# Kernel optimization log

Measured on AMD Instinct MI355X. Metric: run time of the kernel, lower is better.

The kernel has to match this reference:

```python
import jax, jax.numpy as jnp
import numpy as np

MAX_NUM_CAPS = 10
NEG = -1e9

def _layernorm(x, g, b):
    m = x.mean(-1, keepdims=True)
    v = x.var(-1, keepdims=True)
    return (x - m) / jnp.sqrt(v + 1e-5) * g + b

def _gatv2(x, Wl, Wr, att, bias, adj):
    # x: [B,M,F]; Wl/Wr: [F,H*C]; att: [H,C]; adj: [B,M,M] bool, adj[b,i,j] = edge i->j
    B, M, F = x.shape
    H, C = att.shape
    xl = jnp.einsum('bmf,fhc->bmhc', x, Wl.reshape(F, H, C))  # source transform
    xr = jnp.einsum('bmf,fhc->bmhc', x, Wr.reshape(F, H, C))  # target transform
    # GATv2 score: att . leaky_relu(xl[i] + xr[j]) for edge (src=i, dst=j)
    z = jax.nn.leaky_relu(xl[:, :, None, :, :] + xr[:, None, :, :, :], 0.2)  # [B,i,j,H,C]
    e = jnp.einsum('bijhc,hc->bijh', z, att)
    e = jnp.where(adj[..., None], e, NEG)
    alpha = jax.nn.softmax(e, axis=1)  # softmax over incoming sources i per target j
    out = jnp.einsum('bijh,bihc->bjhc', alpha, xl)  # aggregate at targets
    return out.reshape(B, M, H * C) + bias

def setup_inputs() -> dict:
    key = jax.random.key(0)
    ks = jax.random.split(key, 16)
    B, N, T = 128, 16, 48
    Fm, H, C3 = 128, 4, 64
    s = 0.05
    inp = {
        'team_obs': jax.random.normal(ks[0], (B, N, 14), jnp.float32),
        'target_obs': jax.random.normal(ks[1], (B, T, 15), jnp.float32),
        'team_mask': jax.random.normal(ks[2], (B, 2, N), jnp.float32),
        'local_target_mask': jnp.ones((B, T + 1), jnp.float32),
        'W_emb': jax.random.normal(ks[3], (16, Fm), jnp.float32) * s,
        'b_emb': jnp.zeros((Fm,), jnp.float32),
        'Wl1': jax.random.normal(ks[4], (Fm, Fm), jnp.float32) * s,
        'Wr1': jax.random.normal(ks[5], (Fm, Fm), jnp.float32) * s,
        'att1': jax.random.normal(ks[6], (H, Fm // H), jnp.float32) * s,
        'b1': jnp.zeros((Fm,), jnp.float32),
        'Wl2': jax.random.normal(ks[7], (Fm, Fm), jnp.float32) * s,
        'Wr2': jax.random.normal(ks[8], (Fm, Fm), jnp.float32) * s,
        'att2': jax.random.normal(ks[9], (H, Fm // H), jnp.float32) * s,
        'b2': jnp.zeros((Fm,), jnp.float32),
        'Wl3': jax.random.normal(ks[10], (Fm, C3), jnp.float32) * s,
        'Wr3': jax.random.normal(ks[11], (Fm, C3), jnp.float32) * s,
        'att3': jax.random.normal(ks[12], (1, C3), jnp.float32) * s,
        'b3': jnp.zeros((C3,), jnp.float32),
        'ln1_g': jnp.ones((Fm,), jnp.float32),
        'ln1_b': jnp.zeros((Fm,), jnp.float32),
        'ln2_g': jnp.ones((Fm,), jnp.float32),
        'ln2_b': jnp.zeros((Fm,), jnp.float32),
    }
    return inp

def reference(team_obs, target_obs, team_mask, local_target_mask,
              W_emb, b_emb, Wl1, Wr1, att1, b1, Wl2, Wr2, att2, b2,
              Wl3, Wr3, att3, b3, ln1_g, ln1_b, ln2_g, ln2_b):
    B, N, _ = team_obs.shape
    team = jnp.concatenate([team_obs, jnp.zeros((B, N, 2), team_obs.dtype)], axis=2)
    tgt = target_obs[:, :, :-1]
    T = tgt.shape[1]
    tgt = jnp.concatenate([tgt[:, :, :2 + MAX_NUM_CAPS],
                           jnp.zeros((B, T, 2), tgt.dtype),
                           tgt[:, :, -2:]], axis=2)
    fin = jnp.concatenate([team, tgt], axis=1)  # [B, M, inp_dim]
    h = fin @ W_emb + b_emb  # [B, M, 128]
    imp_team = team_mask[:, 0] != -1e9          # [B, N]
    imp_tgt = local_target_mask[:, :-1] != 0.0  # [B, T]
    imp = jnp.concatenate([imp_team, imp_tgt], axis=1)  # [B, M]
    M = N + T
    eye = jnp.eye(M, dtype=bool)
    # edges among active nodes minus diagonal; PyG GATv2Conv add_self_loops=True re-adds self edges
    adj = (imp[:, :, None] & imp[:, None, :] & ~eye) | eye  # [B, M, M]
    out = jax.nn.relu(_layernorm(_gatv2(h, Wl1, Wr1, att1, b1, adj), ln1_g, ln1_b))
    out = jax.nn.relu(_layernorm(_gatv2(out, Wl2, Wr2, att2, b2, adj), ln2_g, ln2_b))
    out = _gatv2(out, Wl3, Wr3, att3, b3, adj)
    return out  # [B, M, out_dim]
```

## Files before the change

### kernel.cpp

```cpp
#include <hip/hip_runtime.h>

typedef unsigned short u16;
typedef unsigned int   u32;
typedef _Float16 h2  __attribute__((ext_vector_type(2)));
typedef __fp16   hw2 __attribute__((ext_vector_type(2)));

#define XS 136

static __device__ __forceinline__ h2 pk(float a, float b) {
    return __builtin_bit_cast(h2, __builtin_amdgcn_cvt_pkrtz(a, b));
}
static __device__ __forceinline__ float dot2(h2 a, h2 b, float c) {
    return __builtin_amdgcn_fdot2(__builtin_bit_cast(hw2, a),
                                  __builtin_bit_cast(hw2, b), c, false);
}
static __device__ __forceinline__ h2  b2h(u32 v) { return __builtin_bit_cast(h2, v); }
static __device__ __forceinline__ u32 h2u(h2 v)  { return __builtin_bit_cast(u32, v); }
static __device__ __forceinline__ h2  abs2(h2 v) { return b2h(h2u(v) & 0x7fff7fffu); }
static __device__ __forceinline__ u16 f2h(float f) { return __builtin_bit_cast(u16, (_Float16)f); }
static __device__ __forceinline__ float h2f(u16 v) { return (float)__builtin_bit_cast(_Float16, v); }

__global__ void pack_weights(const float* __restrict__ Wl1, const float* __restrict__ Wr1,
                             const float* __restrict__ Wl2, const float* __restrict__ Wr2,
                             const float* __restrict__ Wl3, const float* __restrict__ Wr3,
                             u32* __restrict__ wpk)
{
    const int blk = blockIdx.x, t = threadIdx.x;
    const float* src; u32* dst; int local; int sh;
    if      (blk < 32)  { src = Wl1; dst = wpk;         local = blk*256 + t;       sh = 7; }
    else if (blk < 64)  { src = Wr1; dst = wpk + 8192;  local = (blk-32)*256 + t;  sh = 7; }
    else if (blk < 96)  { src = Wl2; dst = wpk + 16384; local = (blk-64)*256 + t;  sh = 7; }
    else if (blk < 128) { src = Wr2; dst = wpk + 24576; local = (blk-96)*256 + t;  sh = 7; }
    else if (blk < 144) { src = Wl3; dst = wpk + 32768; local = (blk-128)*256 + t; sh = 6; }
    else                { src = Wr3; dst = wpk + 36864; local = (blk-144)*256 + t; sh = 6; }
    const int N  = 1 << sh;
    const int k2 = local >> sh;
    const int n  = local & (N - 1);
    float a = src[(2*k2)*N + n];
    float b = src[(2*k2+1)*N + n];
    dst[local] = h2u(pk(a, b));
}

static __device__ __forceinline__ void gat_layer(
    int t, int w, int lane,
    const u32* __restrict__ wpkL, const u32* __restrict__ wpkR,
    const float* __restrict__ att, const float* __restrict__ bias,
    const float* __restrict__ lg, const float* __restrict__ lb,
    u16* sX, u16* sXl, u16* sXrT, float* sAl, float* sPart, float* sL2, const float* sImp)
{
    {
        const int n = t & 127;
        const int g = t >> 7;
        float accL[16], accR[16];
#pragma unroll
        for (int q = 0; q < 16; q++) { accL[q] = 0.f; accR[q] = 0.f; }
        for (int kb = 0; kb < 16; kb++) {
            h2 wl2[4], wr2[4];
#pragma unroll
            for (int q = 0; q < 4; q++) {
                int k2 = kb*4 + q;
                wl2[q] = b2h(wpkL[k2*128 + n]);
                wr2[q] = b2h(wpkR[k2*128 + n]);
            }
#pragma unroll
            for (int mm = 0; mm < 16; mm++) {
                int m = g*16 + mm;
                uint4 v = *(const uint4*)&sX[m*XS + kb*8];
                h2 x0 = b2h(v.x), x1 = b2h(v.y), x2 = b2h(v.z), x3 = b2h(v.w);
                accL[mm] = dot2(x0, wl2[0], accL[mm]);
                accL[mm] = dot2(x1, wl2[1], accL[mm]);
                accL[mm] = dot2(x2, wl2[2], accL[mm]);
                accL[mm] = dot2(x3, wl2[3], accL[mm]);
                accR[mm] = dot2(x0, wr2[0], accR[mm]);
                accR[mm] = dot2(x1, wr2[1], accR[mm]);
                accR[mm] = dot2(x2, wr2[2], accR[mm]);
                accR[mm] = dot2(x3, wr2[3], accR[mm]);
            }
        }
#pragma unroll
        for (int mm = 0; mm < 16; mm++) {
            int m = g*16 + mm;
            sXl[m*XS + n]  = f2h(accL[mm]);
            sXrT[n*65 + m] = f2h(accR[mm]);
        }
    }
    __syncthreads();

    const int h     = w & 3;
    const int ihalf = w >> 2;
    const int j     = lane;

    h2 a2[16];
#pragma unroll
    for (int q = 0; q < 16; q++) a2[q] = pk(att[h*32 + 2*q], att[h*32 + 2*q + 1]);

    if (w < 4) {
        const uint4* pr = (const uint4*)&sXl[lane*XS + h*32];
        float al = 0.f;
#pragma unroll
        for (int c4 = 0; c4 < 4; c4++) {
            uint4 v = pr[c4];
            al = dot2(b2h(v.x), a2[c4*4+0], al);
            al = dot2(b2h(v.y), a2[c4*4+1], al);
            al = dot2(b2h(v.z), a2[c4*4+2], al);
            al = dot2(b2h(v.w), a2[c4*4+3], al);
        }
        sAl[h*64 + lane] = al;
    }

    h2 xr2[16];
#pragma unroll
    for (int q = 0; q < 16; q++) {
        int c = h*32 + 2*q;
        u16 r0 = sXrT[c*65 + j];
        u16 r1 = sXrT[(c+1)*65 + j];
        xr2[q] = b2h((u32)r0 | ((u32)r1 << 16));
    }
    float Ar = 0.f;
#pragma unroll
    for (int q = 0; q < 16; q++) Ar = dot2(a2[q], xr2[q], Ar);
    const float impj = sImp[j];
    __syncthreads();

    float l = 0.f;
    h2 acc2[16];
#pragma unroll
    for (int q = 0; q < 16; q++) acc2[q] = b2h(0u);
    const int i0 = ihalf * 32;
#pragma unroll 4
    for (int ii = 0; ii < 32; ii++) {
        int i = i0 + ii;
        const uint4* pl = (const uint4*)&sXl[i*XS + h*32];
        uint4 v0 = pl[0], v1 = pl[1], v2 = pl[2], v3 = pl[3];
        h2 xl2[16];
        xl2[0] = b2h(v0.x); xl2[1] = b2h(v0.y); xl2[2]  = b2h(v0.z); xl2[3]  = b2h(v0.w);
        xl2[4] = b2h(v1.x); xl2[5] = b2h(v1.y); xl2[6]  = b2h(v1.z); xl2[7]  = b2h(v1.w);
        xl2[8] = b2h(v2.x); xl2[9] = b2h(v2.y); xl2[10] = b2h(v2.z); xl2[11] = b2h(v2.w);
        xl2[12]= b2h(v3.x); xl2[13]= b2h(v3.y); xl2[14] = b2h(v3.z); xl2[15] = b2h(v3.w);
        float S0 = 0.f, S1 = 0.f;
#pragma unroll
        for (int q = 0; q < 16; q += 2) {
            h2 t0 = abs2(xl2[q]   + xr2[q]);
            h2 t1 = abs2(xl2[q+1] + xr2[q+1]);
            S0 = dot2(a2[q],   t0, S0);
            S1 = dot2(a2[q+1], t1, S1);
        }
        float e  = 0.6f*(sAl[h*64 + i] + Ar) + 0.4f*(S0 + S1);
        float ad = (i == j) ? 1.f : impj * sImp[i];
        float p  = (ad != 0.f) ? __expf(e) : 0.f;
        l += p;
        h2 p2 = pk(p, p);
#pragma unroll
        for (int q = 0; q < 16; q++) acc2[q] += p2 * xl2[q];
    }

    u32* ov = (u32*)sX;
    if (w >= 4) {
        uint4* d4 = (uint4*)(ov + (h*64 + j)*16);
        uint4 o;
        o.x = h2u(acc2[0]);  o.y = h2u(acc2[1]);  o.z = h2u(acc2[2]);  o.w = h2u(acc2[3]);  d4[0] = o;
        o.x = h2u(acc2[4]);  o.y = h2u(acc2[5]);  o.z = h2u(acc2[6]);  o.w = h2u(acc2[7]);  d4[1] = o;
        o.x = h2u(acc2[8]);  o.y = h2u(acc2[9]);  o.z = h2u(acc2[10]); o.w = h2u(acc2[11]); d4[2] = o;
        o.x = h2u(acc2[12]); o.y = h2u(acc2[13]); o.z = h2u(acc2[14]); o.w = h2u(acc2[15]); d4[3] = o;
        sL2[h*64 + j] = l;
    }
    __syncthreads();

    float yv[32];
    if (w < 4) {
        const uint4* s4 = (const uint4*)(ov + (h*64 + j)*16);
        uint4 u0 = s4[0], u1 = s4[1], u2 = s4[2], u3 = s4[3];
        h2 oth[16];
        oth[0] = b2h(u0.x); oth[1] = b2h(u0.y); oth[2]  = b2h(u0.z); oth[3]  = b2h(u0.w);
        oth[4] = b2h(u1.x); oth[5] = b2h(u1.y); oth[6]  = b2h(u1.z); oth[7]  = b2h(u1.w);
        oth[8] = b2h(u2.x); oth[9] = b2h(u2.y); oth[10] = b2h(u2.z); oth[11] = b2h(u2.w);
        oth[12]= b2h(u3.x); oth[13]= b2h(u3.y); oth[14] = b2h(u3.z); oth[15] = b2h(u3.w);
        l += sL2[h*64 + j];
        const float rl = 1.f / l;
        float s1 = 0.f, s2v = 0.f;
#pragma unroll
        for (int q = 0; q < 16; q++) {
            h2 sum = acc2[q] + oth[q];
            float y0 = fmaf((float)sum[0], rl, bias[h*32 + 2*q]);
            float y1 = fmaf((float)sum[1], rl, bias[h*32 + 2*q + 1]);
            yv[2*q] = y0; yv[2*q+1] = y1;
            s1 += y0 + y1;
            s2v = fmaf(y0, y0, s2v);
            s2v = fmaf(y1, y1, s2v);
        }
        sPart[h*64 + j]       = s1;
        sPart[256 + h*64 + j] = s2v;
    }
    __syncthreads();

    if (w < 4) {
        float su = sPart[j] + sPart[64 + j] + sPart[128 + j] + sPart[192 + j];
        float sq = sPart[256 + j] + sPart[320 + j] + sPart[384 + j] + sPart[448 + j];
        const float mean = su * 0.0078125f;
        const float var  = sq * 0.0078125f - mean*mean;
        const float rstd = rsqrtf(var + 1e-5f);
        u32* xd = (u32*)&sX[j*XS + h*32];
#pragma unroll
        for (int q = 0; q < 16; q++) {
            int f0 = h*32 + 2*q;
            float v0 = fmaxf(fmaf((yv[2*q]   - mean)*rstd, lg[f0],   lb[f0]),   0.f);
            float v1 = fmaxf(fmaf((yv[2*q+1] - mean)*rstd, lg[f0+1], lb[f0+1]), 0.f);
            xd[q] = h2u(pk(v0, v1));
        }
    }
    __syncthreads();
}

__global__ void __launch_bounds__(512, 2) GNN_61040075210810_kernel(
    const float* __restrict__ team_obs, const float* __restrict__ target_obs,
    const float* __restrict__ team_mask, const float* __restrict__ local_target_mask,
    const float* __restrict__ W_emb, const float* __restrict__ b_emb,
    const float* __restrict__ att1, const float* __restrict__ b1,
    const float* __restrict__ att2, const float* __restrict__ b2,
    const float* __restrict__ att3, const float* __restrict__ b3,
    const float* __restrict__ ln1_g, const float* __restrict__ ln1_b,
    const float* __restrict__ ln2_g, const float* __restrict__ ln2_b,
    const u32* __restrict__ wpk,
    float* __restrict__ out)
{
    __shared__ __align__(16) u16 sX  [64*XS];
    __shared__ __align__(16) u16 sXl [64*XS];
    __shared__ __align__(16) u16 sXrT[128*65];
    __shared__ float sFin[1024];
    __shared__ float sAl [256];
    __shared__ float sPart[512];
    __shared__ float sL2 [256];
    __shared__ float sImp[64];

    const int t    = threadIdx.x;
    const int w    = t >> 6;
    const int lane = t & 63;
    const int b    = blockIdx.x;

    if (t < 64) {
        float im;
        if (t < 16) im = (team_mask[b*32 + t] != -1000000000.0f) ? 1.f : 0.f;
        else        im = (local_target_mask[b*49 + (t-16)] != 0.0f) ? 1.f : 0.f;
        sImp[t] = im;
    }
    for (int ee = t; ee < 1024; ee += 512) {
        int m = ee >> 4, k = ee & 15;
        float v = 0.f;
        if (m < 16) {
            if (k < 14) v = team_obs[(b*16 + m)*14 + k];
        } else {
            const float* tg = target_obs + (size_t)(b*48 + (m-16))*15;
            if      (k < 12)  v = tg[k];
            else if (k == 14) v = tg[12];
            else if (k == 15) v = tg[13];
        }
        sFin[m*16 + k] = v;
    }
    __syncthreads();

    {
        const int f = t & 127;
        const int g = t >> 7;
        float wreg[16];
#pragma unroll
        for (int k = 0; k < 16; k++) wreg[k] = W_emb[k*128 + f];
        const float bf = b_emb[f];
#pragma unroll
        for (int mm = 0; mm < 16; mm++) {
            int m = g*16 + mm;
            const float4* pf = (const float4*)&sFin[m*16];
            float4 f0 = pf[0], f1 = pf[1], f2 = pf[2], f3 = pf[3];
            float acc = bf;
            acc = fmaf(f0.x, wreg[0],  acc); acc = fmaf(f0.y, wreg[1],  acc);
            acc = fmaf(f0.z, wreg[2],  acc); acc = fmaf(f0.w, wreg[3],  acc);
            acc = fmaf(f1.x, wreg[4],  acc); acc = fmaf(f1.y, wreg[5],  acc);
            acc = fmaf(f1.z, wreg[6],  acc); acc = fmaf(f1.w, wreg[7],  acc);
            acc = fmaf(f2.x, wreg[8],  acc); acc = fmaf(f2.y, wreg[9],  acc);
            acc = fmaf(f2.z, wreg[10], acc); acc = fmaf(f2.w, wreg[11], acc);
            acc = fmaf(f3.x, wreg[12], acc); acc = fmaf(f3.y, wreg[13], acc);
            acc = fmaf(f3.z, wreg[14], acc); acc = fmaf(f3.w, wreg[15], acc);
            sX[m*XS + f] = f2h(acc);
        }
    }
    __syncthreads();

    gat_layer(t, w, lane, wpk,         wpk + 8192,  att1, b1, ln1_g, ln1_b,
              sX, sXl, sXrT, sAl, sPart, sL2, sImp);
    gat_layer(t, w, lane, wpk + 16384, wpk + 24576, att2, b2, ln2_g, ln2_b,
              sX, sXl, sXrT, sAl, sPart, sL2, sImp);

    {
        const int col = t & 63;
        const int isR = (t >> 6) & 1;
        const int g   = t >> 7;
        const u32* wp = isR ? (wpk + 36864) : (wpk + 32768);
        float acc[16];
#pragma unroll
        for (int q = 0; q < 16; q++) acc[q] = 0.f;
        for (int kb = 0; kb < 16; kb++) {
            h2 w2[4];
#pragma unroll
            for (int q = 0; q < 4; q++) w2[q] = b2h(wp[(kb*4 + q)*64 + col]);
#pragma unroll
            for (int mm = 0; mm < 16; mm++) {
                int m = g*16 + mm;
                uint4 v = *(const uint4*)&sX[m*XS + kb*8];
                acc[mm] = dot2(b2h(v.x), w2[0], acc[mm]);
                acc[mm] = dot2(b2h(v.y), w2[1], acc[mm]);
                acc[mm] = dot2(b2h(v.z), w2[2], acc[mm]);
                acc[mm] = dot2(b2h(v.w), w2[3], acc[mm]);
            }
        }
#pragma unroll
        for (int mm = 0; mm < 16; mm++) {
            int m = g*16 + mm;
            if (isR) sXrT[col*65 + m] = f2h(acc[mm]);
            else     sXl[m*XS + col]  = f2h(acc[mm]);
        }
    }
    __syncthreads();

    {
        h2 a2l[4];
#pragma unroll
        for (int q = 0; q < 4; q++) a2l[q] = pk(att3[w*8 + 2*q], att3[w*8 + 2*q + 1]);
        uint4 v = *(const uint4*)&sXl[lane*XS + w*8];
        float al = 0.f;
        al = dot2(b2h(v.x), a2l[0], al);
        al = dot2(b2h(v.y), a2l[1], al);
        al = dot2(b2h(v.z), a2l[2], al);
        al = dot2(b2h(v.w), a2l[3], al);
        sPart[w*64 + lane] = al;
    }
    __syncthreads();
    if (t < 64) {
        sAl[t] = ((sPart[t] + sPart[64+t]) + (sPart[128+t] + sPart[192+t]))
               + ((sPart[256+t] + sPart[320+t]) + (sPart[384+t] + sPart[448+t]));
    }
    __syncthreads();

    const int j = lane;
    u16* sE = &sXrT[64*65];

    {
        h2 a3[32], xr3[32];
#pragma unroll
        for (int q = 0; q < 32; q++) a3[q] = pk(att3[2*q], att3[2*q + 1]);
#pragma unroll
        for (int q = 0; q < 32; q++) {
            u16 r0 = sXrT[(2*q)*65 + j];
            u16 r1 = sXrT[(2*q + 1)*65 + j];
            xr3[q] = b2h((u32)r0 | ((u32)r1 << 16));
        }
        float Ar = 0.f;
#pragma unroll
        for (int q = 0; q < 32; q++) Ar = dot2(a3[q], xr3[q], Ar);
        const float impj = sImp[j];
        const int i0 = w*8;
        for (int ii = 0; ii < 8; ii++) {
            int i = i0 + ii;
            const uint4* pl = (const uint4*)&sXl[i*XS];
            float S0 = 0.f, S1 = 0.f;
#pragma unroll
            for (int c4 = 0; c4 < 8; c4++) {
                uint4 v = pl[c4];
                S0 = dot2(a3[c4*4+0], abs2(b2h(v.x) + xr3[c4*4+0]), S0);
                S1 = dot2(a3[c4*4+1], abs2(b2h(v.y) + xr3[c4*4+1]), S1);
                S0 = dot2(a3[c4*4+2], abs2(b2h(v.z) + xr3[c4*4+2]), S0);
                S1 = dot2(a3[c4*4+3], abs2(b2h(v.w) + xr3[c4*4+3]), S1);
            }
            float e  = 0.6f*(sAl[i] + Ar) + 0.4f*(S0 + S1);
            float ad = (i == j) ? 1.f : impj * sImp[i];
            e = (ad != 0.f) ? e : -60000.0f;
            sE[i*64 + j] = f2h(e);
        }
    }
    __syncthreads();

    {
        const int c0 = w*8;
        h2 acc2[4];
#pragma unroll
        for (int q = 0; q < 4; q++) acc2[q] = b2h(0u);
        float l = 0.f;
        for (int i = 0; i < 64; i++) {
            float p = __expf(h2f(sE[i*64 + j]));
            l += p;
            h2 p2 = pk(p, p);
            uint4 v = *(const uint4*)&sXl[i*XS + c0];
            acc2[0] += p2 * b2h(v.x);
            acc2[1] += p2 * b2h(v.y);
            acc2[2] += p2 * b2h(v.z);
            acc2[3] += p2 * b2h(v.w);
        }
        const float rl = 1.f / l;
        float o[8];
#pragma unroll
        for (int q = 0; q < 4; q++) {
            o[2*q]   = fmaf((float)acc2[q][0], rl, b3[c0 + 2*q]);
            o[2*q+1] = fmaf((float)acc2[q][1], rl, b3[c0 + 2*q + 1]);
        }
        float4* po = (float4*)(out + (size_t)b*4096 + j*64 + c0);
        po[0] = *(const float4*)&o[0];
        po[1] = *(const float4*)&o[4];
    }
}

extern "C" void kernel_launch(void* const* d_in, const int* in_sizes, int n_in,
                              void* d_out, int out_size, void* d_ws, size_t ws_size,
                              hipStream_t stream) {
    (void)in_sizes; (void)n_in; (void)ws_size; (void)out_size;
    const float* team_obs          = (const float*)d_in[0];
    const float* target_obs        = (const float*)d_in[1];
    const float* team_mask         = (const float*)d_in[2];
    const float* local_target_mask = (const float*)d_in[3];
    const float* W_emb             = (const float*)d_in[4];
    const float* b_emb             = (const float*)d_in[5];
    const float* Wl1               = (const float*)d_in[6];
    const float* Wr1               = (const float*)d_in[7];
    const float* att1              = (const float*)d_in[8];
    const float* b1                = (const float*)d_in[9];
    const float* Wl2               = (const float*)d_in[10];
    const float* Wr2               = (const float*)d_in[11];
    const float* att2              = (const float*)d_in[12];
    const float* b2                = (const float*)d_in[13];
    const float* Wl3               = (const float*)d_in[14];
    const float* Wr3               = (const float*)d_in[15];
    const float* att3              = (const float*)d_in[16];
    const float* b3                = (const float*)d_in[17];
    const float* ln1_g             = (const float*)d_in[18];
    const float* ln1_b             = (const float*)d_in[19];
    const float* ln2_g             = (const float*)d_in[20];
    const float* ln2_b             = (const float*)d_in[21];
    float* out = (float*)d_out;
    u32*   wpk = (u32*)d_ws;

    pack_weights<<<dim3(160), dim3(256), 0, stream>>>(Wl1, Wr1, Wl2, Wr2, Wl3, Wr3, wpk);
    GNN_61040075210810_kernel<<<dim3(128), dim3(512), 0, stream>>>(
        team_obs, target_obs, team_mask, local_target_mask, W_emb, b_emb,
        att1, b1, att2, b2, att3, b3, ln1_g, ln1_b, ln2_g, ln2_b, wpk, out);
}
```

Baseline: 161.8 us.

## Use MFMA 16x16x32 f16 for GAT linear projections with fragment-packed weights

Result: faster. 144.8 us (-10.5%).

```diff
diff --git a/kernel.cpp b/kernel.cpp
--- a/kernel.cpp
+++ b/kernel.cpp
@@ -4,6 +4,8 @@
 typedef unsigned int   u32;
 typedef _Float16 h2  __attribute__((ext_vector_type(2)));
 typedef __fp16   hw2 __attribute__((ext_vector_type(2)));
+typedef __fp16   hw8 __attribute__((ext_vector_type(8)));
+typedef float    f4  __attribute__((ext_vector_type(4)));
 
 #define XS 136
 
@@ -19,26 +21,32 @@
 static __device__ __forceinline__ h2  abs2(h2 v) { return b2h(h2u(v) & 0x7fff7fffu); }
 static __device__ __forceinline__ u16 f2h(float f) { return __builtin_bit_cast(u16, (_Float16)f); }
 static __device__ __forceinline__ float h2f(u16 v) { return (float)__builtin_bit_cast(_Float16, v); }
+static __device__ __forceinline__ f4 mfma16(uint4 a, uint4 b, f4 c) {
+    return __builtin_amdgcn_mfma_f32_16x16x32_f16(__builtin_bit_cast(hw8, a),
+                                                  __builtin_bit_cast(hw8, b), c, 0, 0, 0);
+}
 
 __global__ void pack_weights(const float* __restrict__ Wl1, const float* __restrict__ Wr1,
                              const float* __restrict__ Wl2, const float* __restrict__ Wr2,
                              const float* __restrict__ Wl3, const float* __restrict__ Wr3,
                              u32* __restrict__ wpk)
 {
-    const int blk = blockIdx.x, t = threadIdx.x;
-    const float* src; u32* dst; int local; int sh;
-    if      (blk < 32)  { src = Wl1; dst = wpk;         local = blk*256 + t;       sh = 7; }
-    else if (blk < 64)  { src = Wr1; dst = wpk + 8192;  local = (blk-32)*256 + t;  sh = 7; }
-    else if (blk < 96)  { src = Wl2; dst = wpk + 16384; local = (blk-64)*256 + t;  sh = 7; }
-    else if (blk < 128) { src = Wr2; dst = wpk + 24576; local = (blk-96)*256 + t;  sh = 7; }
-    else if (blk < 144) { src = Wl3; dst = wpk + 32768; local = (blk-128)*256 + t; sh = 6; }
-    else                { src = Wr3; dst = wpk + 36864; local = (blk-144)*256 + t; sh = 6; }
-    const int N  = 1 << sh;
-    const int k2 = local >> sh;
-    const int n  = local & (N - 1);
-    float a = src[(2*k2)*N + n];
-    float b = src[(2*k2+1)*N + n];
-    dst[local] = h2u(pk(a, b));
+    const int o = blockIdx.x * 256 + threadIdx.x;
+    const float* src; u32* dst; int local; int N;
+    if      (o < 8192)  { src = Wl1; dst = wpk;         local = o;         N = 128; }
+    else if (o < 16384) { src = Wr1; dst = wpk + 8192;  local = o - 8192;  N = 128; }
+    else if (o < 24576) { src = Wl2; dst = wpk + 16384; local = o - 16384; N = 128; }
+    else if (o < 32768) { src = Wr2; dst = wpk + 24576; local = o - 24576; N = 128; }
+    else if (o < 36864) { src = Wl3; dst = wpk + 32768; local = o - 32768; N = 64;  }
+    else                { src = Wr3; dst = wpk + 36864; local = o - 36864; N = 64;  }
+    const int i2   = local & 3;
+    const int lane = (local >> 2) & 63;
+    const int frag = local >> 8;
+    const int kb   = frag & 3;
+    const int nt   = frag >> 2;
+    const int k0   = kb*32 + ((lane >> 4) << 3) + i2*2;
+    const int n    = nt*16 + (lane & 15);
+    dst[local] = h2u(pk(src[k0*N + n], src[(k0+1)*N + n]));
 }
 
 static __device__ __forceinline__ void gat_layer(
@@ -46,42 +54,37 @@
     const u32* __restrict__ wpkL, const u32* __restrict__ wpkR,
     const float* __restrict__ att, const float* __restrict__ bias,
     const float* __restrict__ lg, const float* __restrict__ lb,
-    u16* sX, u16* sXl, u16* sXrT, float* sAl, float* sPart, float* sL2, const float* sImp)
+    u16* sX, u16* sXl, uint4* sXrP, float* sAl, float* sPart, float* sL2, const float* sImp)
 {
     {
-        const int n = t & 127;
-        const int g = t >> 7;
-        float accL[16], accR[16];
-#pragma unroll
-        for (int q = 0; q < 16; q++) { accL[q] = 0.f; accR[q] = 0.f; }
-        for (int kb = 0; kb < 16; kb++) {
-            h2 wl2[4], wr2[4];
-#pragma unroll
-            for (int q = 0; q < 4; q++) {
-                int k2 = kb*4 + q;
-                wl2[q] = b2h(wpkL[k2*128 + n]);
-                wr2[q] = b2h(wpkR[k2*128 + n]);
+        const int  mt  = w & 3;
+        const bool isR = (w >= 4);
+        const u32* wp  = isR ? wpkR : wpkL;
+        const int  n15 = lane & 15;
+        const int  qd  = lane >> 4;
+        uint4 afr[4];
+#pragma unroll
+        for (int kb = 0; kb < 4; kb++)
+            afr[kb] = *(const uint4*)&sX[(mt*16 + n15)*XS + kb*32 + (qd << 3)];
+#pragma unroll
+        for (int nt = 0; nt < 8; nt++) {
+            f4 acc = {0.f, 0.f, 0.f, 0.f};
+#pragma unroll
+            for (int kb = 0; kb < 4; kb++) {
+                uint4 bf = *(const uint4*)&wp[((nt*4 + kb)*64 + lane)*4];
+                acc = mfma16(afr[kb], bf, acc);
             }
-#pragma unroll
-            for (int mm = 0; mm < 16; mm++) {
-                int m = g*16 + mm;
-                uint4 v = *(const uint4*)&sX[m*XS + kb*8];
-                h2 x0 = b2h(v.x), x1 = b2h(v.y), x2 = b2h(v.z), x3 = b2h(v.w);
-                accL[mm] = dot2(x0, wl2[0], accL[mm]);
-                accL[mm] = dot2(x1, wl2[1], accL[mm]);
-                accL[mm] = dot2(x2, wl2[2], accL[mm]);
-                accL[mm] = dot2(x3, wl2[3], accL[mm]);
-                accR[mm] = dot2(x0, wr2[0], accR[mm]);
-                accR[mm] = dot2(x1, wr2[1], accR[mm]);
-                accR[mm] = dot2(x2, wr2[2], accR[mm]);
-                accR[mm] = dot2(x3, wr2[3], accR[mm]);
+            const int n  = nt*16 + n15;
+            const int mb = mt*16 + (qd << 2);
+            if (!isR) {
+#pragma unroll
+                for (int r = 0; r < 4; r++) sXl[(mb + r)*XS + n] = f2h(acc[r]);
+            } else {
+                u16* xp = (u16*)sXrP;
+#pragma unroll
+                for (int r = 0; r < 4; r++)
+                    xp[(((n >> 3)*64) + mb + r)*8 + (n & 7)] = f2h(acc[r]);
             }
-        }
-#pragma unroll
-        for (int mm = 0; mm < 16; mm++) {
-            int m = g*16 + mm;
-            sXl[m*XS + n]  = f2h(accL[mm]);
-            sXrT[n*65 + m] = f2h(accR[mm]);
         }
     }
     __syncthreads();
@@ -110,11 +113,10 @@
 
     h2 xr2[16];
 #pragma unroll
-    for (int q = 0; q < 16; q++) {
-        int c = h*32 + 2*q;
-        u16 r0 = sXrT[c*65 + j];
-        u16 r1 = sXrT[(c+1)*65 + j];
-        xr2[q] = b2h((u32)r0 | ((u32)r1 << 16));
+    for (int s = 0; s < 4; s++) {
+        uint4 v = sXrP[(h*4 + s)*64 + j];
+        xr2[s*4+0] = b2h(v.x); xr2[s*4+1] = b2h(v.y);
+        xr2[s*4+2] = b2h(v.z); xr2[s*4+3] = b2h(v.w);
     }
     float Ar = 0.f;
 #pragma unroll
@@ -223,9 +225,9 @@
     const u32* __restrict__ wpk,
     float* __restrict__ out)
 {
-    __shared__ __align__(16) u16 sX  [64*XS];
-    __shared__ __align__(16) u16 sXl [64*XS];
-    __shared__ __align__(16) u16 sXrT[128*65];
+    __shared__ __align__(16) u16   sX  [64*XS];
+    __shared__ __align__(16) u16   sXl [64*XS];
+    __shared__ __align__(16) uint4 sXrP[1024];
     __shared__ float sFin[1024];
     __shared__ float sAl [256];
     __shared__ float sPart[512];
@@ -285,37 +287,39 @@
     __syncthreads();
 
     gat_layer(t, w, lane, wpk,         wpk + 8192,  att1, b1, ln1_g, ln1_b,
-              sX, sXl, sXrT, sAl, sPart, sL2, sImp);
+              sX, sXl, sXrP, sAl, sPart, sL2, sImp);
     gat_layer(t, w, lane, wpk + 16384, wpk + 24576, att2, b2, ln2_g, ln2_b,
-              sX, sXl, sXrT, sAl, sPart, sL2, sImp);
-
-    {
-        const int col = t & 63;
-        const int isR = (t >> 6) & 1;
-        const int g   = t >> 7;
-        const u32* wp = isR ? (wpk + 36864) : (wpk + 32768);
-        float acc[16];
-#pragma unroll
-        for (int q = 0; q < 16; q++) acc[q] = 0.f;
-        for (int kb = 0; kb < 16; kb++) {
-            h2 w2[4];
-#pragma unroll
-            for (int q = 0; q < 4; q++) w2[q] = b2h(wp[(kb*4 + q)*64 + col]);
-#pragma unroll
-            for (int mm = 0; mm < 16; mm++) {
-                int m = g*16 + mm;
-                uint4 v = *(const uint4*)&sX[m*XS + kb*8];
-                acc[mm] = dot2(b2h(v.x), w2[0], acc[mm]);
-                acc[mm] = dot2(b2h(v.y), w2[1], acc[mm]);
-                acc[mm] = dot2(b2h(v.z), w2[2], acc[mm]);
-                acc[mm] = dot2(b2h(v.w), w2[3], acc[mm]);
+              sX, sXl, sXrP, sAl, sPart, sL2, sImp);
+
+    {
+        const int  mt  = w & 3;
+        const bool isR = (w >= 4);
+        const u32* wp  = isR ? (wpk + 36864) : (wpk + 32768);
+        const int  n15 = lane & 15;
+        const int  qd  = lane >> 4;
+        uint4 afr[4];
+#pragma unroll
+        for (int kb = 0; kb < 4; kb++)
+            afr[kb] = *(const uint4*)&sX[(mt*16 + n15)*XS + kb*32 + (qd << 3)];
+#pragma unroll
+        for (int nt = 0; nt < 4; nt++) {
+            f4 acc = {0.f, 0.f, 0.f, 0.f};
+#pragma unroll
+            for (int kb = 0; kb < 4; kb++) {
+                uint4 bf = *(const uint4*)&wp[((nt*4 + kb)*64 + lane)*4];
+                acc = mfma16(afr[kb], bf, acc);
             }
-        }
-#pragma unroll
-        for (int mm = 0; mm < 16; mm++) {
-            int m = g*16 + mm;
-            if (isR) sXrT[col*65 + m] = f2h(acc[mm]);
-            else     sXl[m*XS + col]  = f2h(acc[mm]);
+            const int n  = nt*16 + n15;
+            const int mb = mt*16 + (qd << 2);
+            if (!isR) {
+#pragma unroll
+                for (int r = 0; r < 4; r++) sXl[(mb + r)*XS + n] = f2h(acc[r]);
+            } else {
+                u16* xp = (u16*)sXrP;
+#pragma unroll
+                for (int r = 0; r < 4; r++)
+                    xp[(((n >> 3)*64) + mb + r)*8 + (n & 7)] = f2h(acc[r]);
+            }
         }
     }
     __syncthreads();
@@ -340,17 +344,17 @@
     __syncthreads();
 
     const int j = lane;
-    u16* sE = &sXrT[64*65];
+    u16* sE = (u16*)sX;
 
     {
         h2 a3[32], xr3[32];
 #pragma unroll
         for (int q = 0; q < 32; q++) a3[q] = pk(att3[2*q], att3[2*q + 1]);
 #pragma unroll
-        for (int q = 0; q < 32; q++) {
-            u16 r0 = sXrT[(2*q)*65 + j];
-            u16 r1 = sXrT[(2*q + 1)*65 + j];
-            xr3[q] = b2h((u32)r0 | ((u32)r1 << 16));
+        for (int s = 0; s < 8; s++) {
+            uint4 v = sXrP[s*64 + j];
+            xr3[s*4+0] = b2h(v.x); xr3[s*4+1] = b2h(v.y);
+            xr3[s*4+2] = b2h(v.z); xr3[s*4+3] = b2h(v.w);
         }
         float Ar = 0.f;
 #pragma unroll
```
